# Kernel optimization log

Hardware: AMD Instinct MI355X
Metric: run time of the kernel (lower is better)

The kernel has to match this reference:

```python
import jax, jax.numpy as jnp
import numpy as np
import math

B, S, D, H, L, DFF = 32, 512, 1024, 16, 4, 4096
DK = D // H  # 64


def setup_inputs() -> dict:
    key = jax.random.key(0)
    ks = jax.random.split(key, 8)
    sc = 0.02
    w = lambda k, shp: (jax.random.normal(k, shp, jnp.float32) * sc)
    return dict(
        q_embed_data=jax.random.normal(ks[0], (B, S, D), jnp.float32),
        qa_embed_data=jax.random.normal(ks[1], (B, S, D), jnp.float32),
        Wk=w(ks[2], (L, D, D)), bk=jnp.zeros((L, D), jnp.float32),
        Wv=w(ks[3], (L, D, D)), bv=jnp.zeros((L, D), jnp.float32),
        Wo=w(ks[4], (L, D, D)), bo=jnp.zeros((L, D), jnp.float32),
        g1=jnp.ones((L, D), jnp.float32), be1=jnp.zeros((L, D), jnp.float32),
        W1=w(ks[5], (L, D, DFF)), c1=jnp.zeros((L, DFF), jnp.float32),
        W2=w(ks[6], (L, DFF, D)), c2=jnp.zeros((L, D), jnp.float32),
        g2=jnp.ones((L, D), jnp.float32), be2=jnp.zeros((L, D), jnp.float32),
    )


def _posemb(seqlen, d_model):
    # sinusoidal table (the 0.1*randn init is fully overwritten since d_model is even)
    pos = jnp.arange(seqlen, dtype=jnp.float32)[:, None]
    div = jnp.exp(jnp.arange(0, d_model, 2, dtype=jnp.float32) * (-math.log(10000.0) / d_model))
    pe = jnp.zeros((seqlen, d_model), jnp.float32)
    pe = pe.at[:, 0::2].set(jnp.sin(pos * div)).at[:, 1::2].set(jnp.cos(pos * div))
    return pe


def _ln(x, g, b, eps=1e-5):
    m = jnp.mean(x, axis=-1, keepdims=True)
    v = jnp.mean(jnp.square(x - m), axis=-1, keepdims=True)
    return (x - m) * jax.lax.rsqrt(v + eps) * g + b


def reference(q_embed_data, qa_embed_data, Wk, bk, Wv, bv, Wo, bo,
              g1, be1, W1, c1, W2, c2, g2, be2):
    pe = _posemb(S, D)
    x = q_embed_data + pe          # query/key stream
    y = qa_embed_data + pe         # value stream (constant across blocks)
    idx = jnp.arange(S)
    allowed = idx[:, None] > idx[None, :]  # strictly-past: triu(k=0) masked incl. diagonal

    def block(x, p):
        Wk_, bk_, Wv_, bv_, Wo_, bo_, g1_, be1_, W1_, c1_, W2_, c2_, g2_, be2_ = p
        # kq_same=1: q and k both use k_linear
        qh = (x @ Wk_ + bk_).reshape(B, S, H, DK).transpose(0, 2, 1, 3)
        kh = qh
        vh = (y @ Wv_ + bv_).reshape(B, S, H, DK).transpose(0, 2, 1, 3)
        scores = jnp.einsum('bhid,bhjd->bhij', qh, kh) / math.sqrt(DK)
        attn = jax.nn.softmax(jnp.where(allowed, scores, -1e32), axis=-1)
        # zero_pad trick: row 0 of attention is replaced by zeros
        attn = attn.at[:, :, 0, :].set(0.0)
        out = jnp.einsum('bhij,bhjd->bhid', attn, vh)
        out = out.transpose(0, 2, 1, 3).reshape(B, S, D) @ Wo_ + bo_
        x = _ln(x + out, g1_, be1_)
        ffn = jax.nn.relu(x @ W1_ + c1_) @ W2_ + c2_
        x = _ln(x + ffn, g2_, be2_)
        return x, None

    x, _ = jax.lax.scan(block, x, (Wk, bk, Wv, bv, Wo, bo, g1, be1, W1, c1, W2, c2, g2, be2))
    return x
```

## Files before the change

### kernel.cpp

```cpp
#include <hip/hip_runtime.h>


#define DEV static __device__ __forceinline__

typedef unsigned short u16;
typedef __attribute__((ext_vector_type(4))) unsigned short u16x4;
typedef __attribute__((ext_vector_type(8))) unsigned short u16x8;
typedef __attribute__((ext_vector_type(8))) short bf16x8;
typedef __attribute__((ext_vector_type(4))) float f32x4;

static constexpr int Bn = 32, Sn = 512, Dn = 1024, Hn = 16, Ln = 4, DFFn = 4096, DKn = 64;
static constexpr int Mn = Bn * Sn;

DEV u16 f2bf(float f) {
  unsigned u = __float_as_uint(f);
  u += 0x7FFFu + ((u >> 16) & 1u);
  return (u16)(u >> 16);
}
DEV float bf2f(u16 v) { return __uint_as_float((unsigned)v << 16); }

DEV void gload_lds16(const void* g, void* l) {
  __builtin_amdgcn_global_load_lds((const __attribute__((address_space(1))) void*)g,
                                   (__attribute__((address_space(3))) void*)l, 16, 0, 0);
}

DEV void barf() {
  asm volatile("" ::: "memory");
  __builtin_amdgcn_s_barrier();
  asm volatile("" ::: "memory");
}

__global__ __launch_bounds__(256) void pe_add_kernel(
    const float* __restrict__ q, const float* __restrict__ qa,
    float* __restrict__ x, u16* __restrict__ xb, u16* __restrict__ yb)
{
  size_t i4 = ((size_t)blockIdx.x * 256 + threadIdx.x) * 4;
  int d0 = (int)(i4 & (Dn - 1));
  int s  = (int)((i4 >> 10) & (Sn - 1));
  float p = (float)s;
  const float LC = 0.0089944730195f;
  float a0 = p * expf(-LC * (float)d0);
  float a2 = p * expf(-LC * (float)(d0 + 2));
  float pe0 = sinf(a0), pe1 = cosf(a0), pe2 = sinf(a2), pe3 = cosf(a2);
  const float4 qv = *(const float4*)(q + i4);
  const float4 av = *(const float4*)(qa + i4);
  float x0 = qv.x + pe0, x1 = qv.y + pe1, x2 = qv.z + pe2, x3 = qv.w + pe3;
  float y0 = av.x + pe0, y1 = av.y + pe1, y2 = av.z + pe2, y3 = av.w + pe3;
  *(float4*)(x + i4) = make_float4(x0, x1, x2, x3);
  u16x4 xv4 = { f2bf(x0), f2bf(x1), f2bf(x2), f2bf(x3) };
  u16x4 yv4 = { f2bf(y0), f2bf(y1), f2bf(y2), f2bf(y3) };
  *(u16x4*)(xb + i4) = xv4;
  *(u16x4*)(yb + i4) = yv4;
}

__global__ __launch_bounds__(256) void transpose_cast_kernel(
    const float* __restrict__ in, u16* __restrict__ out, int R, int C)
{
  __shared__ float t[32][33];
  int tx = threadIdx.x & 31, ty = threadIdx.x >> 5;
  int c0 = blockIdx.x * 32, r0 = blockIdx.y * 32;
  #pragma unroll
  for (int i = 0; i < 4; ++i)
    t[ty + i * 8][tx] = in[(size_t)(r0 + ty + i * 8) * C + c0 + tx];
  __syncthreads();
  #pragma unroll
  for (int i = 0; i < 4; ++i) {
    int rr = ty + i * 8;
    out[(size_t)(c0 + rr) * R + r0 + tx] = f2bf(t[tx][rr]);
  }
}

__global__ __launch_bounds__(256) void transpose_cast3_kernel(
    const float* __restrict__ i0, const float* __restrict__ i1, const float* __restrict__ i2,
    u16* __restrict__ o0, u16* __restrict__ o1, u16* __restrict__ o2)
{
  const int z = blockIdx.z;
  const float* in = (z == 0) ? i0 : (z == 1) ? i1 : i2;
  u16* out = (z == 0) ? o0 : (z == 1) ? o1 : o2;
  __shared__ float t[32][33];
  int tx = threadIdx.x & 31, ty = threadIdx.x >> 5;
  int c0 = blockIdx.x * 32, r0 = blockIdx.y * 32;
  #pragma unroll
  for (int i = 0; i < 4; ++i)
    t[ty + i * 8][tx] = in[(size_t)(r0 + ty + i * 8) * Dn + c0 + tx];
  __syncthreads();
  #pragma unroll
  for (int i = 0; i < 4; ++i) {
    int rr = ty + i * 8;
    out[(size_t)(c0 + rr) * Dn + r0 + tx] = f2bf(t[tx][rr]);
  }
}

__global__ __launch_bounds__(256) void vtrans_kernel(const u16* __restrict__ V, u16* __restrict__ Vt)
{
  __shared__ u16 t[64][72];
  const int idx = blockIdx.x;
  const int st = idx & 7, h = (idx >> 3) & 15, b = idx >> 7;
  const int s0 = st * 64;
  const int tid = threadIdx.x;
  const int r = tid >> 3, c8 = (tid & 7) * 8;
  #pragma unroll
  for (int p = 0; p < 2; ++p) {
    int row = r + 32 * p;
    *(u16x8*)&t[row][c8] = *(const u16x8*)&V[(size_t)(b * Sn + s0 + row) * Dn + h * DKn + c8];
  }
  __syncthreads();
  #pragma unroll
  for (int p = 0; p < 2; ++p) {
    int drow = r + 32 * p;
    u16x8 w;
    #pragma unroll
    for (int j = 0; j < 8; ++j) w[j] = t[c8 + j][drow];
    *(u16x8*)&Vt[((size_t)((b * Hn + h) * DKn + drow) << 9) + s0 + c8] = w;
  }
}

template<int BIAS, int RELU, int F32OUT, int ACC, int DUAL = 0>
__global__ __launch_bounds__(512, 2) void gemm8p_kernel(
    const u16* __restrict__ A, int lda,
    const u16* __restrict__ BT, int ldb,
    const float* __restrict__ bias,
    void* __restrict__ Cout, int ldc,
    int M, int N, int K,
    const u16* A2 = nullptr, const u16* BT2 = nullptr,
    const float* bias2 = nullptr, void* Cout2 = nullptr)
{
  if (DUAL && blockIdx.z) { A = A2; BT = BT2; bias = bias2; Cout = Cout2; }
  __shared__ u16 lds[2][2][16384];
  const int tid = threadIdx.x;
  const int lane = tid & 63, wid = tid >> 6;
  const int g = lane >> 4, r16 = lane & 15;
  const int wm = wid >> 2, wn = wid & 3;

  const int nwgx = N >> 8;
  const int nwg = gridDim.x * gridDim.y;
  const int flat = blockIdx.y * gridDim.x + blockIdx.x;
  const int cpx = nwg >> 3;
  const int logical = (flat & 7) * cpx + (flat >> 3);
  const int n0 = (logical % nwgx) << 8;
  const int m0 = (logical / nwgx) << 8;

  f32x4 acc[8][4];
  #pragma unroll
  for (int i = 0; i < 8; ++i)
    #pragma unroll
    for (int j = 0; j < 4; ++j) acc[i][j] = (f32x4){0.f, 0.f, 0.f, 0.f};

  const int rr = tid >> 3, ck = tid & 7;
  const int scol = ((ck ^ (rr & 7)) << 3);
  const u16* Asrc = A  + (size_t)(m0 + rr) * lda + scol;
  const u16* Bsrc = BT + (size_t)(n0 + rr) * ldb + scol;
  const int eds = rr * 64 + ck * 8;
  const size_t a64 = (size_t)64 * lda, b64 = (size_t)64 * ldb;

  #define STG(p, h, t) do {                                                  \
    if ((h) < 2) {                                                           \
      const u16* s_ = Asrc + (size_t)((h) * 128) * lda + (t) * 64;           \
      gload_lds16(s_,       &lds[p][0][eds + (h) * 8192]);                   \
      gload_lds16(s_ + a64, &lds[p][0][eds + (h) * 8192 + 4096]);            \
    } else {                                                                 \
      const u16* s_ = Bsrc + (size_t)(((h) - 2) * 128) * ldb + (t) * 64;     \
      gload_lds16(s_,       &lds[p][1][eds + ((h) - 2) * 8192]);             \
      gload_lds16(s_ + b64, &lds[p][1][eds + ((h) - 2) * 8192 + 4096]);      \
    }                                                                        \
  } while (0)

  const int c0 = ((g ^ (r16 & 7)) << 3);
  const int c1 = (((4 + g) ^ (r16 & 7)) << 3);
  const int arow = wm * 128 + r16;
  const int brow = wn * 64 + r16;

  #define LDA2(p, q, af) do {                                                        \
    af[0][0] = *(const bf16x8*)&lds[p][0][(arow + (2*(q))   * 16) * 64 + c0];        \
    af[0][1] = *(const bf16x8*)&lds[p][0][(arow + (2*(q))   * 16) * 64 + c1];        \
    af[1][0] = *(const bf16x8*)&lds[p][0][(arow + (2*(q)+1) * 16) * 64 + c0];        \
    af[1][1] = *(const bf16x8*)&lds[p][0][(arow + (2*(q)+1) * 16) * 64 + c1];        \
  } while (0)

  #define MMQ(q, af, bf) do {                                                        \
    __builtin_amdgcn_s_setprio(1);                                                   \
    _Pragma("unroll")                                                                \
    for (int ks = 0; ks < 2; ++ks)                                                   \
      _Pragma("unroll")                                                              \
      for (int i2 = 0; i2 < 2; ++i2)                                                 \
        _Pragma("unroll")                                                            \
        for (int j = 0; j < 4; ++j)                                                  \
          acc[2*(q)+i2][j] = __builtin_amdgcn_mfma_f32_16x16x32_bf16(af[i2][ks], bf[j][ks], acc[2*(q)+i2][j], 0, 0, 0); \
    __builtin_amdgcn_s_setprio(0);                                                   \
  } while (0)

  const int nt = K >> 6;
  STG(0, 0, 0); STG(0, 1, 0); STG(0, 2, 0); STG(0, 3, 0);
  if (nt > 1) {
    STG(1, 0, 1);
    asm volatile("s_waitcnt vmcnt(2)" ::: "memory");
  } else {
    asm volatile("s_waitcnt vmcnt(0)" ::: "memory");
  }
  barf();

  for (int t = 0; t < nt; ++t) {
    const int p = t & 1;
    bf16x8 bf[4][2], af[2][2];
    #pragma unroll
    for (int j = 0; j < 4; ++j) {
      bf[j][0] = *(const bf16x8*)&lds[p][1][(brow + j * 16) * 64 + c0];
      bf[j][1] = *(const bf16x8*)&lds[p][1][(brow + j * 16) * 64 + c1];
    }
    LDA2(p, 0, af);
    if (t + 1 < nt) { STG(p ^ 1, 1, t + 1); STG(p ^ 1, 2, t + 1); }
    barf();
    MMQ(0, af, bf);
    LDA2(p, 1, af);
    if (t + 1 < nt) STG(p ^ 1, 3, t + 1);
    barf();
    MMQ(1, af, bf);
    LDA2(p, 2, af);
    barf();
    MMQ(2, af, bf);
    LDA2(p, 3, af);
    asm volatile("s_waitcnt lgkmcnt(0)" ::: "memory");
    barf();
    if (t + 2 < nt) STG(p, 0, t + 2);
    MMQ(3, af, bf);
    if (t + 2 < nt) {
      asm volatile("s_waitcnt vmcnt(2)" ::: "memory");
    } else {
      asm volatile("s_waitcnt vmcnt(0)" ::: "memory");
    }
    barf();
  }
  #undef STG
  #undef LDA2
  #undef MMQ

  #pragma unroll
  for (int i = 0; i < 8; ++i) {
    const int rb = m0 + wm * 128 + i * 16 + 4 * g;
    #pragma unroll
    for (int j = 0; j < 4; ++j) {
      const int col = n0 + wn * 64 + j * 16 + r16;
      float badd = BIAS ? bias[col] : 0.f;
      #pragma unroll
      for (int r = 0; r < 4; ++r) {
        size_t off = (size_t)(rb + r) * ldc + col;
        float v = acc[i][j][r] + badd;
        if (RELU) v = fmaxf(v, 0.f);
        if (F32OUT) {
          float* Cf = (float*)Cout;
          if (ACC) v += Cf[off];
          Cf[off] = v;
        } else {
          ((u16*)Cout)[off] = f2bf(v);
        }
      }
    }
  }
}

__global__ __launch_bounds__(512) void fattn_kernel(
    const u16* __restrict__ Kb, const u16* __restrict__ Vt, u16* __restrict__ O)
{
  __shared__ u16 kl[64][72];
  __shared__ u16 vl[64][72];
  __shared__ u16 pw[8][16][72];
  const int idx = blockIdx.x;
  const int qt = idx & 3;
  const int h  = (idx >> 2) & 15;
  const int b  = idx >> 6;
  const int Q0 = qt * 128;
  const int tid = threadIdx.x;
  const int lane = tid & 63, w = tid >> 6;
  const int g = lane >> 4, r16 = lane & 15;
  const int myrow = Q0 + 16 * w;

  bf16x8 qf[2];
  {
    const u16* qrow = &Kb[(size_t)(b * Sn + myrow + r16) * Dn + h * DKn];
    qf[0] = *(const bf16x8*)(qrow + 8 * g);
    qf[1] = *(const bf16x8*)(qrow + 32 + 8 * g);
  }
  f32x4 oacc[4];
  float mrow[4], lrow[4];
  #pragma unroll
  for (int j = 0; j < 4; ++j) oacc[j] = (f32x4){0.f, 0.f, 0.f, 0.f};
  #pragma unroll
  for (int r = 0; r < 4; ++r) { mrow[r] = -1e30f; lrow[r] = 0.f; }

  const int srow = tid >> 3;
  const int scol = (tid & 7) * 8;
  const u16* kbase = Kb + (size_t)(b * Sn) * Dn + h * DKn;
  const u16* vbase = Vt + (size_t)(b * Hn + h) * DKn * Sn;
  const int ctmax = 2 * qt + 1;

  for (int ct = 0; ct <= ctmax; ++ct) {
    __syncthreads();
    *(u16x8*)&kl[srow][scol] = *(const u16x8*)&kbase[(size_t)(ct * 64 + srow) * Dn + scol];
    *(u16x8*)&vl[srow][scol] = *(const u16x8*)&vbase[(size_t)srow * Sn + ct * 64 + scol];
    __syncthreads();
    if (ct * 64 > myrow + 14) continue;

    f32x4 sa[4];
    #pragma unroll
    for (int j = 0; j < 4; ++j) {
      sa[j] = (f32x4){0.f, 0.f, 0.f, 0.f};
      #pragma unroll
      for (int ks = 0; ks < 2; ++ks) {
        bf16x8 kf = *(const bf16x8*)&kl[16 * j + r16][32 * ks + 8 * g];
        sa[j] = __builtin_amdgcn_mfma_f32_16x16x32_bf16(qf[ks], kf, sa[j], 0, 0, 0);
      }
    }
    const bool needmask = (ct * 64 + 63 >= myrow);
    float p4[4][4];
    #pragma unroll
    for (int j = 0; j < 4; ++j)
      #pragma unroll
      for (int r = 0; r < 4; ++r) {
        float v = sa[j][r] * 0.125f;
        if (needmask && (ct * 64 + 16 * j + r16 >= myrow + 4 * g + r)) v = -3e38f;
        p4[j][r] = v;
      }
    #pragma unroll
    for (int r = 0; r < 4; ++r) {
      float m = fmaxf(fmaxf(p4[0][r], p4[1][r]), fmaxf(p4[2][r], p4[3][r]));
      #pragma unroll
      for (int o = 8; o; o >>= 1) m = fmaxf(m, __shfl_xor(m, o));
      float mn = fmaxf(mrow[r], m);
      float sc = __expf(mrow[r] - mn);
      mrow[r] = mn;
      float s = 0.f;
      #pragma unroll
      for (int j = 0; j < 4; ++j) {
        float e = __expf(p4[j][r] - mn);
        p4[j][r] = e;
        s += e;
      }
      #pragma unroll
      for (int o = 8; o; o >>= 1) s += __shfl_xor(s, o);
      lrow[r] = lrow[r] * sc + s;
      #pragma unroll
      for (int j = 0; j < 4; ++j) oacc[j][r] *= sc;
    }
    #pragma unroll
    for (int j = 0; j < 4; ++j)
      #pragma unroll
      for (int r = 0; r < 4; ++r)
        pw[w][4 * g + r][16 * j + r16] = f2bf(p4[j][r]);
    #pragma unroll
    for (int ks = 0; ks < 2; ++ks) {
      bf16x8 pa = *(const bf16x8*)&pw[w][r16][32 * ks + 8 * g];
      #pragma unroll
      for (int j = 0; j < 4; ++j) {
        bf16x8 vb = *(const bf16x8*)&vl[16 * j + r16][32 * ks + 8 * g];
        oacc[j] = __builtin_amdgcn_mfma_f32_16x16x32_bf16(pa, vb, oacc[j], 0, 0, 0);
      }
    }
  }
  #pragma unroll
  for (int r = 0; r < 4; ++r) {
    float inv = (lrow[r] > 0.f) ? 1.f / lrow[r] : 0.f;
    #pragma unroll
    for (int j = 0; j < 4; ++j)
      O[(size_t)(b * Sn + myrow + 4 * g + r) * Dn + h * DKn + 16 * j + r16] =
          f2bf(oacc[j][r] * inv);
  }
}

template<int TBF>
__global__ __launch_bounds__(256) void ln_kernel(
    const float* __restrict__ xin, const void* __restrict__ tin,
    const float* __restrict__ pb, const float* __restrict__ gam,
    const float* __restrict__ bet, float* __restrict__ xout, u16* __restrict__ xbout)
{
  const int row = blockIdx.x;
  const int tid = threadIdx.x;
  const size_t base = (size_t)row * Dn + tid * 4;
  float4 xv = *(const float4*)(xin + base);
  float4 tv;
  if (TBF) {
    u16x4 t4 = *(const u16x4*)((const u16*)tin + base);
    tv = make_float4(bf2f(t4[0]), bf2f(t4[1]), bf2f(t4[2]), bf2f(t4[3]));
  } else {
    tv = *(const float4*)((const float*)tin + base);
  }
  float4 bb = *(const float4*)(pb + tid * 4);
  float v0 = xv.x + tv.x + bb.x, v1 = xv.y + tv.y + bb.y;
  float v2 = xv.z + tv.z + bb.z, v3 = xv.w + tv.w + bb.w;
  float s  = v0 + v1 + v2 + v3;
  float s2 = v0 * v0 + v1 * v1 + v2 * v2 + v3 * v3;
  #pragma unroll
  for (int o = 32; o > 0; o >>= 1) { s += __shfl_xor(s, o); s2 += __shfl_xor(s2, o); }
  __shared__ float rs[4], rs2[4];
  const int wid = tid >> 6;
  if ((tid & 63) == 0) { rs[wid] = s; rs2[wid] = s2; }
  __syncthreads();
  s  = rs[0] + rs[1] + rs[2] + rs[3];
  s2 = rs2[0] + rs2[1] + rs2[2] + rs2[3];
  const float mean = s * (1.f / Dn);
  const float var  = s2 * (1.f / Dn) - mean * mean;
  const float rstd = rsqrtf(fmaxf(var, 0.f) + 1e-5f);
  float4 gv = *(const float4*)(gam + tid * 4);
  float4 bv = *(const float4*)(bet + tid * 4);
  float o0 = (v0 - mean) * rstd * gv.x + bv.x;
  float o1 = (v1 - mean) * rstd * gv.y + bv.y;
  float o2 = (v2 - mean) * rstd * gv.z + bv.z;
  float o3 = (v3 - mean) * rstd * gv.w + bv.w;
  *(float4*)(xout + base) = make_float4(o0, o1, o2, o3);
  u16x4 ub = { f2bf(o0), f2bf(o1), f2bf(o2), f2bf(o3) };
  *(u16x4*)(xbout + base) = ub;
}

extern "C" void kernel_launch(void* const* d_in, const int* in_sizes, int n_in,
                              void* d_out, int out_size, void* d_ws, size_t ws_size,
                              hipStream_t stream)
{
  const float* q   = (const float*)d_in[0];
  const float* qa  = (const float*)d_in[1];
  const float* Wk  = (const float*)d_in[2];
  const float* bk  = (const float*)d_in[3];
  const float* Wv  = (const float*)d_in[4];
  const float* bv  = (const float*)d_in[5];
  const float* Wo  = (const float*)d_in[6];
  const float* bo  = (const float*)d_in[7];
  const float* g1  = (const float*)d_in[8];
  const float* be1 = (const float*)d_in[9];
  const float* W1  = (const float*)d_in[10];
  const float* c1  = (const float*)d_in[11];
  const float* W2  = (const float*)d_in[12];
  const float* c2  = (const float*)d_in[13];
  const float* g2  = (const float*)d_in[14];
  const float* be2 = (const float*)d_in[15];
  float* x = (float*)d_out;

  const size_t MD  = (size_t)Mn * Dn;
  const size_t MF  = (size_t)Mn * DFFn;
  const size_t WSZ = 3 * (size_t)Dn * Dn * 2 + 2 * (size_t)Dn * DFFn * 2;
  const size_t NEED_SMALL = 5 * MD * 2 + WSZ + 8192;
  const size_t NEED_BIG   = 2 * MD * 2 + MF * 2 + MD * 4 + WSZ + 8192;
  if (ws_size < NEED_SMALL) return;
  const bool big = (ws_size >= NEED_BIG);

  char* wsb = (char*)d_ws;
  size_t off = 0;
  auto take = [&](size_t bytes) -> void* {
    void* r = wsb + off;
    off += (bytes + 255) & ~(size_t)255;
    return r;
  };
  u16 *XB, *YB, *KB, *VT, *VB, *H1 = nullptr;
  float* TMP;
  XB = (u16*)take(MD * 2);
  YB = (u16*)take(MD * 2);
  if (big) {
    H1  = (u16*)take(MF * 2);
    TMP = (float*)take(MD * 4);
    KB  = H1;
    VT  = H1 + MD;
    VB  = H1 + 2 * MD;
  } else {
    KB  = (u16*)take(MD * 2);
    VT  = (u16*)take(MD * 2);
    VB  = (u16*)take(MD * 2);
    TMP = (float*)KB;
  }
  u16* WKT = (u16*)take((size_t)Dn * Dn * 2);
  u16* WVT = (u16*)take((size_t)Dn * Dn * 2);
  u16* WOT = (u16*)take((size_t)Dn * Dn * 2);
  u16* W1T = (u16*)take((size_t)Dn * DFFn * 2);
  u16* W2T = (u16*)take((size_t)Dn * DFFn * 2);
  u16* H1C = VB;
  u16* TMPB = (u16*)TMP;
  (void)in_sizes; (void)n_in; (void)out_size;

  pe_add_kernel<<<Mn * Dn / 1024, 256, 0, stream>>>(q, qa, x, XB, YB);

  const dim3 g256(Dn / 256, Mn / 256);
  const dim3 g256z(Dn / 256, Mn / 256, 2);
  const dim3 gW1(DFFn / 256, Mn / 256);
  for (int l = 0; l < Ln; ++l) {
    const size_t wo = (size_t)l * Dn * Dn;
    const size_t fo = (size_t)l * Dn * DFFn;
    transpose_cast3_kernel<<<dim3(32, 32, 3), 256, 0, stream>>>(
        Wk + wo, Wv + wo, Wo + wo, WKT, WVT, WOT);
    transpose_cast_kernel<<<dim3(128, 32), 256, 0, stream>>>(W1 + fo, W1T, Dn, DFFn);
    transpose_cast_kernel<<<dim3(32, 128), 256, 0, stream>>>(W2 + fo, W2T, DFFn, Dn);

    gemm8p_kernel<1,0,0,0,1><<<g256z, 512, 0, stream>>>(
        XB, Dn, WKT, Dn, bk + l * Dn, KB, Dn, Mn, Dn, Dn,
        YB, WVT, bv + l * Dn, VB);
    vtrans_kernel<<<Bn * Hn * 8, 256, 0, stream>>>(VB, VT);
    fattn_kernel<<<Bn * Hn * 4, 512, 0, stream>>>(KB, VT, VB);
    if (big) {
      gemm8p_kernel<0,0,0,0><<<g256, 512, 0, stream>>>(VB, Dn, WOT, Dn, nullptr, TMPB, Dn, Mn, Dn, Dn);
      ln_kernel<1><<<Mn, 256, 0, stream>>>(x, TMPB, bo + l * Dn, g1 + l * Dn, be1 + l * Dn, x, XB);
      gemm8p_kernel<1,1,0,0><<<gW1, 512, 0, stream>>>(
          XB, Dn, W1T, Dn, c1 + l * DFFn, H1, DFFn, Mn, DFFn, Dn);
      gemm8p_kernel<0,0,0,0><<<g256, 512, 0, stream>>>(
          H1, DFFn, W2T, DFFn, nullptr, TMPB, Dn, Mn, Dn, DFFn);
      ln_kernel<1><<<Mn, 256, 0, stream>>>(x, TMPB, c2 + l * Dn, g2 + l * Dn, be2 + l * Dn, x, XB);
    } else {
      gemm8p_kernel<0,0,1,0><<<g256, 512, 0, stream>>>(VB, Dn, WOT, Dn, nullptr, TMP, Dn, Mn, Dn, Dn);
      ln_kernel<0><<<Mn, 256, 0, stream>>>(x, TMP, bo + l * Dn, g1 + l * Dn, be1 + l * Dn, x, XB);
      for (int ci = 0; ci < 4; ++ci) {
        gemm8p_kernel<1,1,0,0><<<g256, 512, 0, stream>>>(
            XB, Dn, W1T + (size_t)ci * Dn * Dn, Dn, c1 + l * DFFn + ci * Dn, H1C, Dn, Mn, Dn, Dn);
        if (ci == 0)
          gemm8p_kernel<0,0,1,0><<<g256, 512, 0, stream>>>(
              H1C, Dn, W2T + (size_t)ci * Dn, DFFn, nullptr, TMP, Dn, Mn, Dn, Dn);
        else
          gemm8p_kernel<0,0,1,1><<<g256, 512, 0, stream>>>(
              H1C, Dn, W2T + (size_t)ci * Dn, DFFn, nullptr, TMP, Dn, Mn, Dn, Dn);
      }
      ln_kernel<0><<<Mn, 256, 0, stream>>>(x, TMP, c2 + l * Dn, g2 + l * Dn, be2 + l * Dn, x, XB);
    }
  }
}
```

Before: 2.218 ms.

## Simplify GEMM main loop to one barrier per K-tile with double-buffered A fragments

Restructures the GEMM K-loop so that each iteration prefetches all four stages of the next tile into the alternate LDS buffer and synchronises with a single barrier at the end, instead of four barriers per iteration. A fragments alternate between two register sets so LDS reads can overlap MFMAs. The two-tile-ahead prefetch of stage 0 and the partial vmcnt waits are removed, so global loads now get only one tile of lead time and each iteration waits on vmcnt(0). Register pressure also rises from the extra fragment set.

```diff
diff --git a/kernel.cpp b/kernel.cpp
--- a/kernel.cpp
+++ b/kernel.cpp
@@ -191,43 +191,31 @@
 
   const int nt = K >> 6;
   STG(0, 0, 0); STG(0, 1, 0); STG(0, 2, 0); STG(0, 3, 0);
-  if (nt > 1) {
-    STG(1, 0, 1);
-    asm volatile("s_waitcnt vmcnt(2)" ::: "memory");
-  } else {
-    asm volatile("s_waitcnt vmcnt(0)" ::: "memory");
-  }
+  asm volatile("s_waitcnt vmcnt(0)" ::: "memory");
   barf();
 
   for (int t = 0; t < nt; ++t) {
     const int p = t & 1;
-    bf16x8 bf[4][2], af[2][2];
+    const bool pf = (t + 1 < nt);
+    bf16x8 bf[4][2], af[2][2], ag[2][2];
     #pragma unroll
     for (int j = 0; j < 4; ++j) {
       bf[j][0] = *(const bf16x8*)&lds[p][1][(brow + j * 16) * 64 + c0];
       bf[j][1] = *(const bf16x8*)&lds[p][1][(brow + j * 16) * 64 + c1];
     }
     LDA2(p, 0, af);
-    if (t + 1 < nt) { STG(p ^ 1, 1, t + 1); STG(p ^ 1, 2, t + 1); }
-    barf();
+    if (pf) { STG(p ^ 1, 0, t + 1); STG(p ^ 1, 1, t + 1); }
     MMQ(0, af, bf);
-    LDA2(p, 1, af);
-    if (t + 1 < nt) STG(p ^ 1, 3, t + 1);
-    barf();
-    MMQ(1, af, bf);
+    LDA2(p, 1, ag);
+    if (pf) STG(p ^ 1, 2, t + 1);
+    MMQ(1, ag, bf);
     LDA2(p, 2, af);
-    barf();
+    if (pf) STG(p ^ 1, 3, t + 1);
     MMQ(2, af, bf);
-    LDA2(p, 3, af);
+    LDA2(p, 3, ag);
+    MMQ(3, ag, bf);
     asm volatile("s_waitcnt lgkmcnt(0)" ::: "memory");
-    barf();
-    if (t + 2 < nt) STG(p, 0, t + 2);
-    MMQ(3, af, bf);
-    if (t + 2 < nt) {
-      asm volatile("s_waitcnt vmcnt(2)" ::: "memory");
-    } else {
-      asm volatile("s_waitcnt vmcnt(0)" ::: "memory");
-    }
+    asm volatile("s_waitcnt vmcnt(0)" ::: "memory");
     barf();
   }
   #undef STG
```

Result: no change. 2.193 ms (-1.1%).
